# Performance work log

Measured on AMD Instinct MI355X. Metric: run time of the kernel, lower is better.

## Reference

```python
import jax, jax.numpy as jnp
import numpy as np

B, T, C, H = 2, 2048, 1024, 16

def setup_inputs() -> dict:
    key = jax.random.key(0)
    k1, k2, k3 = jax.random.split(key, 3)
    scale = 0.02
    return {
        "x": jax.random.normal(k1, (B, T, C), dtype=jnp.float32),
        "w_attn": jax.random.normal(k2, (C, 3 * C), dtype=jnp.float32) * scale,
        "b_attn": jnp.zeros((3 * C,), dtype=jnp.float32),
        "w_proj": jax.random.normal(k3, (C, C), dtype=jnp.float32) * scale,
        "b_proj": jnp.zeros((C,), dtype=jnp.float32),
    }

def reference(x, w_attn, b_attn, w_proj, b_proj):
    Bx, Tx, Cx = x.shape
    hd = Cx // H  # head dim
    qkv = x @ w_attn + b_attn  # [B,T,3C]
    q, k, v = jnp.split(qkv, 3, axis=-1)
    # [B,H,T,hd]
    q = q.reshape(Bx, Tx, H, hd).transpose(0, 2, 1, 3)
    k = k.reshape(Bx, Tx, H, hd).transpose(0, 2, 1, 3)
    v = v.reshape(Bx, Tx, H, hd).transpose(0, 2, 1, 3)
    att = jnp.einsum('bhqd,bhkd->bhqk', q, k) * (1.0 / jnp.sqrt(jnp.float32(hd)))
    causal = jnp.tril(jnp.ones((Tx, Tx), dtype=bool))  # [T,T]
    att = jnp.where(causal[None, None], att, jnp.float32(-jnp.inf))
    att = jax.nn.softmax(att, axis=-1)
    y = jnp.einsum('bhqk,bhkd->bhqd', att, v)  # [B,H,T,hd]
    y = y.transpose(0, 2, 1, 3).reshape(Bx, Tx, Cx)
    return y @ w_proj + b_proj
```

## Files before the change

### kernel.cpp

```cpp
#include <hip/hip_runtime.h>
#include <hip/hip_bf16.h>
#include <stdint.h>

#define B_SZ 2
#define T_SZ 2048
#define C_SZ 1024
#define H_SZ 16
#define HD   64
#define BH   (B_SZ * H_SZ)
#define M_SZ (B_SZ * T_SZ)
#define N_QKV (3 * C_SZ)

typedef __attribute__((ext_vector_type(8))) __bf16 bf16x8;
typedef __attribute__((ext_vector_type(4))) float f32x4;
typedef __attribute__((ext_vector_type(8))) unsigned short us8;
typedef __attribute__((ext_vector_type(4))) unsigned short us4;
typedef __attribute__((ext_vector_type(4))) unsigned int u32x4;

__device__ __forceinline__ unsigned short f2bf(float f) {
    unsigned int u = __builtin_bit_cast(unsigned int, f);
    u += 0x7fffu + ((u >> 16) & 1u);
    return (unsigned short)(u >> 16);
}

__device__ __forceinline__ void gll16(const unsigned short* g, unsigned short* l) {
    __builtin_amdgcn_global_load_lds(
        (const __attribute__((address_space(1))) unsigned int*)g,
        (__attribute__((address_space(3))) unsigned int*)l, 16, 0, 0);
}

__device__ __forceinline__ void hard_sync() {
    asm volatile("s_waitcnt vmcnt(0) lgkmcnt(0)" ::: "memory");
    __builtin_amdgcn_sched_barrier(0);
    __syncthreads();
}

__global__ __launch_bounds__(256) void k_prep(const float* __restrict__ x,
                                              const float* __restrict__ wa,
                                              const float* __restrict__ wp,
                                              unsigned short* __restrict__ xb,
                                              unsigned short* __restrict__ wta,
                                              unsigned short* __restrict__ wtp) {
    __shared__ float tile[32][33];
    const int tid = threadIdx.x;
    int idx = blockIdx.x;
    if (idx < 2048) {
        const size_t i = ((size_t)idx * 256 + tid) * 8;
        f32x4 a = *(const f32x4*)(x + i);
        f32x4 b = *(const f32x4*)(x + i + 4);
        us8 o;
        #pragma unroll
        for (int j = 0; j < 4; ++j) { o[j] = f2bf(a[j]); o[4 + j] = f2bf(b[j]); }
        *(us8*)(xb + i) = o;
        return;
    }
    const float* in; unsigned short* out; int N;
    if (idx < 5120) { idx -= 2048; in = wa; out = wta; N = N_QKV; }
    else            { idx -= 5120; in = wp; out = wtp; N = C_SZ; }
    const int nx = N / 32;
    const int n0 = (idx % nx) * 32, k0 = (idx / nx) * 32;
    const int tx = tid & 31, ty = tid >> 5;
    #pragma unroll
    for (int j = 0; j < 32; j += 8)
        tile[ty + j][tx] = in[(size_t)(k0 + ty + j) * N + (n0 + tx)];
    __syncthreads();
    #pragma unroll
    for (int j = 0; j < 32; j += 8)
        out[(size_t)(n0 + ty + j) * C_SZ + (k0 + tx)] = f2bf(tile[tx][ty + j]);
}

template <int EPI>
__global__ __launch_bounds__(256) void k_gemm(const unsigned short* __restrict__ A,
                                              const unsigned short* __restrict__ Bt,
                                              const float* __restrict__ bias,
                                              float* __restrict__ Cout,
                                              unsigned short* __restrict__ q_ws,
                                              unsigned short* __restrict__ k_ws,
                                              unsigned short* __restrict__ vT_ws,
                                              int M, int N, int K, int NX) {
    __shared__ __attribute__((aligned(16))) unsigned short Ald[128 * 64];
    __shared__ __attribute__((aligned(16))) unsigned short Bld[128 * 64];
    const int tid = threadIdx.x;
    const int wid = tid >> 6, lane = tid & 63;
    const int wr = wid >> 1, wc = wid & 1;
    const int g = lane >> 4, l15 = lane & 15;
    const int nwg = gridDim.x;
    const int wg = (blockIdx.x & 7) * (nwg >> 3) + (blockIdx.x >> 3);
    const int m0 = (wg / NX) * 128, n0 = (wg % NX) * 128;

    f32x4 acc[4][4];
    #pragma unroll
    for (int i = 0; i < 4; ++i)
        #pragma unroll
        for (int j = 0; j < 4; ++j) acc[i][j] = (f32x4){0.f, 0.f, 0.f, 0.f};

    for (int k0 = 0; k0 < K; k0 += 64) {
        hard_sync();
        #pragma unroll
        for (int i = 0; i < 4; ++i) {
            int c = i * 256 + tid;
            int row = c >> 3;
            int colb = ((c & 7) << 4) ^ ((row & 7) << 4);
            gll16(A  + (size_t)(m0 + row) * K + k0 + (colb >> 1), Ald + i * 2048 + wid * 512);
            gll16(Bt + (size_t)(n0 + row) * K + k0 + (colb >> 1), Bld + i * 2048 + wid * 512);
        }
        hard_sync();

        #pragma unroll
        for (int ks = 0; ks < 2; ++ks) {
            bf16x8 af[4], bfr[4];
            #pragma unroll
            for (int mi = 0; mi < 4; ++mi) {
                int row = wr * 64 + mi * 16 + l15;
                af[mi] = *(const bf16x8*)((const char*)Ald + row * 128 +
                                          ((ks * 64 + g * 16) ^ ((row & 7) << 4)));
            }
            #pragma unroll
            for (int nj = 0; nj < 4; ++nj) {
                int row = wc * 64 + nj * 16 + l15;
                bfr[nj] = *(const bf16x8*)((const char*)Bld + row * 128 +
                                           ((ks * 64 + g * 16) ^ ((row & 7) << 4)));
            }
            #pragma unroll
            for (int mi = 0; mi < 4; ++mi)
                #pragma unroll
                for (int nj = 0; nj < 4; ++nj)
                    acc[mi][nj] = __builtin_amdgcn_mfma_f32_16x16x32_bf16(
                        af[mi], bfr[nj], acc[mi][nj], 0, 0, 0);
        }
    }

    if (EPI == 0) {
        #pragma unroll
        for (int nj = 0; nj < 4; ++nj) {
            int col = n0 + wc * 64 + nj * 16 + l15;
            float bv = bias[col];
            #pragma unroll
            for (int mi = 0; mi < 4; ++mi) {
                int rowb = m0 + wr * 64 + mi * 16 + g * 4;
                #pragma unroll
                for (int r = 0; r < 4; ++r)
                    Cout[(size_t)(rowb + r) * N + col] = acc[mi][nj][r] + bv;
            }
        }
    } else {
        #pragma unroll
        for (int nj = 0; nj < 4; ++nj) {
            int col = n0 + wc * 64 + nj * 16 + l15;
            float bv = bias[col];
            int which = col >> 10;
            int c10 = col & 1023;
            int h = c10 >> 6, d = c10 & 63;
            #pragma unroll
            for (int mi = 0; mi < 4; ++mi) {
                #pragma unroll
                for (int r = 0; r < 4; ++r) {
                    int row = m0 + wr * 64 + mi * 16 + g * 4 + r;
                    int bb = row >> 11, t = row & 2047;
                    unsigned short val = f2bf(acc[mi][nj][r] + bv);
                    if (which == 2)
                        vT_ws[((size_t)(bb * H_SZ + h) * HD + d) * T_SZ + t] = val;
                    else
                        (which ? k_ws : q_ws)[((size_t)(bb * H_SZ + h) * T_SZ + t) * HD + d] = val;
                }
            }
        }
    }
}

__global__ __launch_bounds__(512) void k_attn(const unsigned short* __restrict__ q_ws,
                                              const unsigned short* __restrict__ k_ws,
                                              const unsigned short* __restrict__ vT_ws,
                                              unsigned short* __restrict__ y_ws) {
    __shared__ __attribute__((aligned(16))) unsigned short Kbuf[2][8192];
    __shared__ __attribute__((aligned(16))) unsigned short Vbuf[2][8192];
    const int tid = threadIdx.x;
    const int wid = tid >> 6, lane = tid & 63;
    const int g = lane >> 4, l15 = lane & 15;
    const int n = blockIdx.x;
    const int xcd = n & 7, j = (n >> 3) & 7, rk = n >> 6;
    const int bh = xcd + 8 * rk;
    const size_t kv_off = (size_t)bh * T_SZ * HD;
    const unsigned short* Kg = k_ws + kv_off;
    const unsigned short* Vg = vT_ws + (size_t)bh * HD * T_SZ;
    const int b = bh >> 4, h = bh & 15;
    const float SC = 0.125f * 1.44269504f;
    const int qloc = wid * 16 + l15;

    auto stageK = [&](int kv, int buf) {
        #pragma unroll
        for (int i = 0; i < 2; ++i) {
            int c = i * 512 + tid;
            int row = c >> 3;
            int colb = ((c & 7) << 4) ^ ((row & 7) << 4);
            gll16(Kg + (size_t)(kv * 128 + row) * HD + (colb >> 1),
                  &Kbuf[buf][i * 4096 + wid * 512]);
        }
    };
    auto stageV = [&](int kv, int buf) {
        #pragma unroll
        for (int i = 0; i < 2; ++i) {
            int c = i * 512 + tid;
            int row = c >> 4;
            int colb = ((c & 15) << 4) ^ ((row & 15) << 4);
            gll16(Vg + (size_t)row * T_SZ + kv * 128 + (colb >> 1),
                  &Vbuf[buf][i * 4096 + wid * 512]);
        }
    };

    #pragma unroll 1
    for (int phase = 0; phase < 2; ++phase) {
        const int qt = phase ? j : (15 - j);
        const int nkv = qt + 1;

        const int qrow = qt * 128 + wid * 16 + l15;
        bf16x8 aq[2];
        aq[0] = *(const bf16x8*)(q_ws + kv_off + (size_t)qrow * HD + g * 8);
        aq[1] = *(const bf16x8*)(q_ws + kv_off + (size_t)qrow * HD + 32 + g * 8);

        float m_run = -3e38f, l_part = 0.f;
        f32x4 acc[4];
        #pragma unroll
        for (int dt = 0; dt < 4; ++dt) acc[dt] = (f32x4){0.f, 0.f, 0.f, 0.f};

        hard_sync();
        stageK(0, 0); stageV(0, 0);
        int cur = 0;

        for (int kv = 0; kv < nkv; ++kv) {
            hard_sync();
            if (kv + 1 < nkv) { stageK(kv + 1, cur ^ 1); stageV(kv + 1, cur ^ 1); }
            const char* Kb = (const char*)Kbuf[cur];
            const char* Vb = (const char*)Vbuf[cur];

            f32x4 st[8];
            __builtin_amdgcn_s_setprio(1);
            #pragma unroll
            for (int kt = 0; kt < 8; ++kt) {
                f32x4 sv = (f32x4){0.f, 0.f, 0.f, 0.f};
                #pragma unroll
                for (int ks = 0; ks < 2; ++ks) {
                    int row = kt * 16 + l15;
                    bf16x8 ak = *(const bf16x8*)(Kb + row * 128 +
                                                 ((ks * 64 + g * 16) ^ ((row & 7) << 4)));
                    sv = __builtin_amdgcn_mfma_f32_16x16x32_bf16(ak, aq[ks], sv, 0, 0, 0);
                }
                st[kt] = sv;
            }
            __builtin_amdgcn_s_setprio(0);

            float t[32];
            #pragma unroll
            for (int kt = 0; kt < 8; ++kt)
                #pragma unroll
                for (int r = 0; r < 4; ++r) t[kt * 4 + r] = st[kt][r];
            if (kv == nkv - 1) {
                const int ql = wid * 16 + l15;
                #pragma unroll
                for (int kt = 0; kt < 8; ++kt)
                    #pragma unroll
                    for (int r = 0; r < 4; ++r)
                        if (kt * 16 + g * 4 + r > ql) t[kt * 4 + r] = -3e38f;
            }

            float m16[16];
            #pragma unroll
            for (int i = 0; i < 16; ++i) m16[i] = fmaxf(t[i], t[i + 16]);
            float m8v[8];
            #pragma unroll
            for (int i = 0; i < 8; ++i) m8v[i] = fmaxf(m16[i], m16[i + 8]);
            float m4v[4];
            #pragma unroll
            for (int i = 0; i < 4; ++i) m4v[i] = fmaxf(m8v[i], m8v[i + 4]);
            float mx = fmaxf(fmaxf(m4v[0], m4v[1]), fmaxf(m4v[2], m4v[3]));
            mx = fmaxf(mx, __shfl_xor(mx, 16, 64));
            mx = fmaxf(mx, __shfl_xor(mx, 32, 64));
            float mt = mx * SC;

            if (!__all(mt - m_run <= 8.0f)) {
                float mnew = fmaxf(m_run, mt);
                float alpha = exp2f(m_run - mnew);
                m_run = mnew;
                l_part *= alpha;
                float ao[4];
                #pragma unroll
                for (int r = 0; r < 4; ++r) {
                    int ai = __builtin_amdgcn_ds_bpermute((g * 4 + r) * 4,
                                                          __builtin_bit_cast(int, alpha));
                    ao[r] = __builtin_bit_cast(float, ai);
                }
                #pragma unroll
                for (int dt = 0; dt < 4; ++dt)
                    #pragma unroll
                    for (int r = 0; r < 4; ++r) acc[dt][r] *= ao[r];
            }

            float p[32];
            #pragma unroll
            for (int i = 0; i < 32; ++i) p[i] = exp2f(fmaf(t[i], SC, -m_run));
            float s16[16];
            #pragma unroll
            for (int i = 0; i < 16; ++i) s16[i] = p[i] + p[i + 16];
            float s8v[8];
            #pragma unroll
            for (int i = 0; i < 8; ++i) s8v[i] = s16[i] + s16[i + 8];
            float s4v[4];
            #pragma unroll
            for (int i = 0; i < 4; ++i) s4v[i] = s8v[i] + s8v[i + 4];
            l_part += (s4v[0] + s4v[1]) + (s4v[2] + s4v[3]);

            unsigned int pk0[8], pk1[8];
            #pragma unroll
            for (int kt = 0; kt < 8; ++kt) {
                asm("v_cvt_pk_bf16_f32 %0, %1, %2" : "=v"(pk0[kt]) : "v"(p[kt * 4 + 0]), "v"(p[kt * 4 + 1]));
                asm("v_cvt_pk_bf16_f32 %0, %1, %2" : "=v"(pk1[kt]) : "v"(p[kt * 4 + 2]), "v"(p[kt * 4 + 3]));
            }
            __builtin_amdgcn_s_setprio(1);
            #pragma unroll
            for (int ks = 0; ks < 4; ++ks) {
                unsigned int x0 = pk0[2 * ks], y0 = pk0[2 * ks + 1];
                unsigned int x1 = pk1[2 * ks], y1 = pk1[2 * ks + 1];
                asm("v_permlane32_swap_b32 %0, %1" : "+v"(x0), "+v"(y0));
                asm("v_permlane16_swap_b32 %0, %1" : "+v"(x0), "+v"(y0));
                asm("v_permlane32_swap_b32 %0, %1" : "+v"(x1), "+v"(y1));
                asm("v_permlane16_swap_b32 %0, %1" : "+v"(x1), "+v"(y1));
                bf16x8 ap = __builtin_bit_cast(bf16x8, (u32x4){x0, x1, y0, y1});
                #pragma unroll
                for (int dt = 0; dt < 4; ++dt) {
                    int row = dt * 16 + l15;
                    bf16x8 bv = *(const bf16x8*)(Vb + row * 256 +
                                                 ((ks * 64 + g * 16) ^ ((row & 15) << 4)));
                    acc[dt] = __builtin_amdgcn_mfma_f32_16x16x32_bf16(ap, bv, acc[dt], 0, 0, 0);
                }
            }
            __builtin_amdgcn_s_setprio(0);
            cur ^= 1;
        }

        float lsum = l_part;
        lsum += __shfl_xor(lsum, 16, 64);
        lsum += __shfl_xor(lsum, 32, 64);
        float lo[4];
        #pragma unroll
        for (int r = 0; r < 4; ++r) {
            int li = __builtin_amdgcn_ds_bpermute((g * 4 + r) * 4,
                                                  __builtin_bit_cast(int, lsum));
            lo[r] = __builtin_bit_cast(float, li);
        }
        #pragma unroll
        for (int r = 0; r < 4; ++r) {
            int tq = qt * 128 + wid * 16 + g * 4 + r;
            float inv = 1.0f / lo[r];
            #pragma unroll
            for (int dt = 0; dt < 4; ++dt)
                y_ws[(size_t)(b * T_SZ + tq) * C_SZ + h * 64 + dt * 16 + l15] =
                    f2bf(acc[dt][r] * inv);
        }
    }
}

extern "C" void kernel_launch(void* const* d_in, const int* in_sizes, int n_in,
                              void* d_out, int out_size, void* d_ws, size_t ws_size,
                              hipStream_t stream) {
    const float* x      = (const float*)d_in[0];
    const float* w_attn = (const float*)d_in[1];
    const float* b_attn = (const float*)d_in[2];
    const float* w_proj = (const float*)d_in[3];
    const float* b_proj = (const float*)d_in[4];
    float* out = (float*)d_out;

    char* ws = (char*)d_ws;
    unsigned short* q_ws  = (unsigned short*)(ws + 0);
    unsigned short* k_ws  = (unsigned short*)(ws + 8388608);
    unsigned short* vT_ws = (unsigned short*)(ws + 16777216);
    unsigned short* wtp   = (unsigned short*)(ws + 25165824);
    unsigned short* xb    = (unsigned short*)(ws + 27262976);
    unsigned short* y_ws  = (unsigned short*)(ws + 27262976);
    unsigned short* wta   = (unsigned short*)(ws + 35651584);

    k_prep<<<dim3(6144), 256, 0, stream>>>(x, w_attn, w_proj, xb, wta, wtp);

    k_gemm<1><<<dim3((N_QKV / 128) * (M_SZ / 128)), 256, 0, stream>>>(
        xb, wta, b_attn, nullptr, q_ws, k_ws, vT_ws, M_SZ, N_QKV, C_SZ, N_QKV / 128);

    k_attn<<<dim3(256), 512, 0, stream>>>(q_ws, k_ws, vT_ws, y_ws);

    k_gemm<0><<<dim3((C_SZ / 128) * (M_SZ / 128)), 256, 0, stream>>>(
        y_ws, wtp, b_proj, out, nullptr, nullptr, nullptr, M_SZ, C_SZ, C_SZ, C_SZ / 128);
}
```

Measured before the change: 118.1 us.

## Software-pipeline attention loop: overlap next QK and softmax with previous PV

Restructures the attention KV loop so each iteration runs QK^T for tile i and PV for tile i-1, then softmax for tile i, using ping-pong packed-probability registers. V staging moves to a triple buffer so the tile read by the delayed PV is not overwritten by the prefetch. The goal is to let the MFMA work of PV interleave with the softmax VALU and exp work, so the matrix units are not idle during the exponentials. In exchange it uses more LDS, which could reduce occupancy, and more live registers across the loop.

```diff
diff --git a/kernel.cpp b/kernel.cpp
--- a/kernel.cpp
+++ b/kernel.cpp
@@ -173,7 +173,7 @@
                                               const unsigned short* __restrict__ vT_ws,
                                               unsigned short* __restrict__ y_ws) {
     __shared__ __attribute__((aligned(16))) unsigned short Kbuf[2][8192];
-    __shared__ __attribute__((aligned(16))) unsigned short Vbuf[2][8192];
+    __shared__ __attribute__((aligned(16))) unsigned short Vbuf[3][8192];
     const int tid = threadIdx.x;
     const int wid = tid >> 6, lane = tid & 63;
     const int g = lane >> 4, l15 = lane & 15;
@@ -222,18 +222,9 @@
         f32x4 acc[4];
         #pragma unroll
         for (int dt = 0; dt < 4; ++dt) acc[dt] = (f32x4){0.f, 0.f, 0.f, 0.f};
-
-        hard_sync();
-        stageK(0, 0); stageV(0, 0);
-        int cur = 0;
-
-        for (int kv = 0; kv < nkv; ++kv) {
-            hard_sync();
-            if (kv + 1 < nkv) { stageK(kv + 1, cur ^ 1); stageV(kv + 1, cur ^ 1); }
-            const char* Kb = (const char*)Kbuf[cur];
-            const char* Vb = (const char*)Vbuf[cur];
-
-            f32x4 st[8];
+        u32x4 pfA[4], pfB[4];
+
+        auto qk = [&](const char* Kb, f32x4 (&st)[8]) {
             __builtin_amdgcn_s_setprio(1);
             #pragma unroll
             for (int kt = 0; kt < 8; ++kt) {
@@ -248,35 +239,48 @@
                 st[kt] = sv;
             }
             __builtin_amdgcn_s_setprio(0);
-
+        };
+        auto pv = [&](const char* Vb, const u32x4 (&pf)[4]) {
+            __builtin_amdgcn_s_setprio(1);
+            #pragma unroll
+            for (int ks = 0; ks < 4; ++ks) {
+                bf16x8 ap = __builtin_bit_cast(bf16x8, pf[ks]);
+                #pragma unroll
+                for (int dt = 0; dt < 4; ++dt) {
+                    int row = dt * 16 + l15;
+                    bf16x8 bv = *(const bf16x8*)(Vb + row * 256 +
+                                                 ((ks * 64 + g * 16) ^ ((row & 15) << 4)));
+                    acc[dt] = __builtin_amdgcn_mfma_f32_16x16x32_bf16(ap, bv, acc[dt], 0, 0, 0);
+                }
+            }
+            __builtin_amdgcn_s_setprio(0);
+        };
+        auto softmax = [&](f32x4 (&st)[8], bool diag, u32x4 (&pf)[4]) {
             float t[32];
             #pragma unroll
             for (int kt = 0; kt < 8; ++kt)
                 #pragma unroll
                 for (int r = 0; r < 4; ++r) t[kt * 4 + r] = st[kt][r];
-            if (kv == nkv - 1) {
-                const int ql = wid * 16 + l15;
+            if (diag) {
                 #pragma unroll
                 for (int kt = 0; kt < 8; ++kt)
                     #pragma unroll
                     for (int r = 0; r < 4; ++r)
-                        if (kt * 16 + g * 4 + r > ql) t[kt * 4 + r] = -3e38f;
-            }
-
-            float m16[16];
-            #pragma unroll
-            for (int i = 0; i < 16; ++i) m16[i] = fmaxf(t[i], t[i + 16]);
+                        if (kt * 16 + g * 4 + r > qloc) t[kt * 4 + r] = -3e38f;
+            }
+            float m16v[16];
+            #pragma unroll
+            for (int i2 = 0; i2 < 16; ++i2) m16v[i2] = fmaxf(t[i2], t[i2 + 16]);
             float m8v[8];
             #pragma unroll
-            for (int i = 0; i < 8; ++i) m8v[i] = fmaxf(m16[i], m16[i + 8]);
+            for (int i2 = 0; i2 < 8; ++i2) m8v[i2] = fmaxf(m16v[i2], m16v[i2 + 8]);
             float m4v[4];
             #pragma unroll
-            for (int i = 0; i < 4; ++i) m4v[i] = fmaxf(m8v[i], m8v[i + 4]);
+            for (int i2 = 0; i2 < 4; ++i2) m4v[i2] = fmaxf(m8v[i2], m8v[i2 + 4]);
             float mx = fmaxf(fmaxf(m4v[0], m4v[1]), fmaxf(m4v[2], m4v[3]));
             mx = fmaxf(mx, __shfl_xor(mx, 16, 64));
             mx = fmaxf(mx, __shfl_xor(mx, 32, 64));
             float mt = mx * SC;
-
             if (!__all(mt - m_run <= 8.0f)) {
                 float mnew = fmaxf(m_run, mt);
                 float alpha = exp2f(m_run - mnew);
@@ -294,48 +298,67 @@
                     #pragma unroll
                     for (int r = 0; r < 4; ++r) acc[dt][r] *= ao[r];
             }
-
             float p[32];
             #pragma unroll
-            for (int i = 0; i < 32; ++i) p[i] = exp2f(fmaf(t[i], SC, -m_run));
-            float s16[16];
-            #pragma unroll
-            for (int i = 0; i < 16; ++i) s16[i] = p[i] + p[i + 16];
+            for (int i2 = 0; i2 < 32; ++i2) p[i2] = exp2f(fmaf(t[i2], SC, -m_run));
+            float s16v[16];
+            #pragma unroll
+            for (int i2 = 0; i2 < 16; ++i2) s16v[i2] = p[i2] + p[i2 + 16];
             float s8v[8];
             #pragma unroll
-            for (int i = 0; i < 8; ++i) s8v[i] = s16[i] + s16[i + 8];
+            for (int i2 = 0; i2 < 8; ++i2) s8v[i2] = s16v[i2] + s16v[i2 + 8];
             float s4v[4];
             #pragma unroll
-            for (int i = 0; i < 4; ++i) s4v[i] = s8v[i] + s8v[i + 4];
+            for (int i2 = 0; i2 < 4; ++i2) s4v[i2] = s8v[i2] + s8v[i2 + 4];
             l_part += (s4v[0] + s4v[1]) + (s4v[2] + s4v[3]);
-
-            unsigned int pk0[8], pk1[8];
-            #pragma unroll
-            for (int kt = 0; kt < 8; ++kt) {
-                asm("v_cvt_pk_bf16_f32 %0, %1, %2" : "=v"(pk0[kt]) : "v"(p[kt * 4 + 0]), "v"(p[kt * 4 + 1]));
-                asm("v_cvt_pk_bf16_f32 %0, %1, %2" : "=v"(pk1[kt]) : "v"(p[kt * 4 + 2]), "v"(p[kt * 4 + 3]));
-            }
-            __builtin_amdgcn_s_setprio(1);
             #pragma unroll
             for (int ks = 0; ks < 4; ++ks) {
-                unsigned int x0 = pk0[2 * ks], y0 = pk0[2 * ks + 1];
-                unsigned int x1 = pk1[2 * ks], y1 = pk1[2 * ks + 1];
+                unsigned int x0, y0, x1, y1;
+                asm("v_cvt_pk_bf16_f32 %0, %1, %2" : "=v"(x0) : "v"(p[8 * ks + 0]), "v"(p[8 * ks + 1]));
+                asm("v_cvt_pk_bf16_f32 %0, %1, %2" : "=v"(x1) : "v"(p[8 * ks + 2]), "v"(p[8 * ks + 3]));
+                asm("v_cvt_pk_bf16_f32 %0, %1, %2" : "=v"(y0) : "v"(p[8 * ks + 4]), "v"(p[8 * ks + 5]));
+                asm("v_cvt_pk_bf16_f32 %0, %1, %2" : "=v"(y1) : "v"(p[8 * ks + 6]), "v"(p[8 * ks + 7]));
                 asm("v_permlane32_swap_b32 %0, %1" : "+v"(x0), "+v"(y0));
                 asm("v_permlane16_swap_b32 %0, %1" : "+v"(x0), "+v"(y0));
                 asm("v_permlane32_swap_b32 %0, %1" : "+v"(x1), "+v"(y1));
                 asm("v_permlane16_swap_b32 %0, %1" : "+v"(x1), "+v"(y1));
-                bf16x8 ap = __builtin_bit_cast(bf16x8, (u32x4){x0, x1, y0, y1});
-                #pragma unroll
-                for (int dt = 0; dt < 4; ++dt) {
-                    int row = dt * 16 + l15;
-                    bf16x8 bv = *(const bf16x8*)(Vb + row * 256 +
-                                                 ((ks * 64 + g * 16) ^ ((row & 15) << 4)));
-                    acc[dt] = __builtin_amdgcn_mfma_f32_16x16x32_bf16(ap, bv, acc[dt], 0, 0, 0);
-                }
-            }
-            __builtin_amdgcn_s_setprio(0);
-            cur ^= 1;
-        }
+                pf[ks] = (u32x4){x0, x1, y0, y1};
+            }
+        };
+
+        hard_sync();
+        stageK(0, 0); stageV(0, 0);
+
+        hard_sync();
+        if (1 < nkv) { stageK(1, 1); stageV(1, 1); }
+        {
+            f32x4 st[8];
+            qk((const char*)Kbuf[0], st);
+            softmax(st, nkv == 1, pfA);
+        }
+        bool lastA = true;
+        for (int i = 1; i < nkv; ) {
+            hard_sync();
+            if (i + 1 < nkv) { stageK(i + 1, (i + 1) & 1); stageV(i + 1, (i + 1) % 3); }
+            {
+                f32x4 st[8];
+                qk((const char*)Kbuf[i & 1], st);
+                pv((const char*)Vbuf[(i - 1) % 3], pfA);
+                softmax(st, i == nkv - 1, pfB);
+            }
+            ++i; lastA = false; if (i == nkv) break;
+            hard_sync();
+            if (i + 1 < nkv) { stageK(i + 1, (i + 1) & 1); stageV(i + 1, (i + 1) % 3); }
+            {
+                f32x4 st[8];
+                qk((const char*)Kbuf[i & 1], st);
+                pv((const char*)Vbuf[(i - 1) % 3], pfB);
+                softmax(st, i == nkv - 1, pfA);
+            }
+            ++i; lastA = true; if (i == nkv) break;
+        }
+        if (lastA) pv((const char*)Vbuf[(nkv - 1) % 3], pfA);
+        else       pv((const char*)Vbuf[(nkv - 1) % 3], pfB);
 
         float lsum = l_part;
         lsum += __shfl_xor(lsum, 16, 64);
```

Measured after the change: 114.0 us. 1.04x faster.
